# Kernel tuning notes

Measured on AMD Instinct MI355X. Metric: run time of the kernel, lower is better.

## Reference

```python
import jax, jax.numpy as jnp
import numpy as np

N_NODES = 100000
N_EDGES = 1600000
NUM_GRAPHS = 256


def _gcn_conv(x, src, dst, deg_isqrt, deg_inv, W, b):
    # GCNConv with self-loops and symmetric normalization (PyG semantics):
    # out_i = sum_{j->i} d_j^-1/2 d_i^-1/2 (x_j W) + d_i^-1 (x_i W) + b
    xl = x @ W  # [N, out]
    norm = deg_isqrt[src] * deg_isqrt[dst]  # [E]
    msgs = norm[:, None] * xl[src]  # [E, out] -- dominant memory traffic
    agg = jax.ops.segment_sum(msgs, dst, num_segments=N_NODES)
    return agg + deg_inv[:, None] * xl + b


def setup_inputs() -> dict:
    key = jax.random.key(0)
    ks = jax.random.split(key, 8)
    F_in, H, T = 128, 128, 64
    x = jax.random.normal(ks[0], (N_NODES, F_in), dtype=jnp.float32)
    edge_index = jax.random.randint(ks[1], (2, N_EDGES), 0, N_NODES, dtype=jnp.int64)
    batch = jnp.sort(jax.random.randint(ks[2], (N_NODES,), 0, NUM_GRAPHS, dtype=jnp.int64))
    s0 = 1.0 / np.sqrt(F_in)
    s1 = 1.0 / np.sqrt(H)
    return {
        "x": x,
        "edge_index": edge_index,
        "batch": batch,
        "W0": jax.random.normal(ks[3], (F_in, H), dtype=jnp.float32) * s0,
        "b0": jnp.zeros((H,), dtype=jnp.float32),
        "W1": jax.random.normal(ks[4], (H, H), dtype=jnp.float32) * s1,
        "b1": jnp.zeros((H,), dtype=jnp.float32),
        "W2": jax.random.normal(ks[5], (H, T), dtype=jnp.float32) * s1,
        "b2": jnp.zeros((T,), dtype=jnp.float32),
    }


def reference(x, edge_index, batch, W0, b0, W1, b1, W2, b2):
    src, dst = edge_index[0], edge_index[1]
    # degree including self-loop
    deg = jax.ops.segment_sum(jnp.ones((N_EDGES,), x.dtype), dst, num_segments=N_NODES) + 1.0
    deg_isqrt = jax.lax.rsqrt(deg)
    deg_inv = 1.0 / deg

    h = jax.nn.gelu(_gcn_conv(x, src, dst, deg_isqrt, deg_inv, W0, b0))
    h = jax.nn.gelu(_gcn_conv(h, src, dst, deg_isqrt, deg_inv, W1, b1))
    h = jax.nn.gelu(_gcn_conv(h, src, dst, deg_isqrt, deg_inv, W2, b2))

    # global_mean_pool over graphs
    sums = jax.ops.segment_sum(h, batch, num_segments=NUM_GRAPHS)
    counts = jax.ops.segment_sum(jnp.ones((N_NODES,), h.dtype), batch, num_segments=NUM_GRAPHS)
    return sums / jnp.maximum(counts, 1.0)[:, None]
```

## Files before the change

### kernel.cpp

```cpp
#include <hip/hip_runtime.h>
#include <math.h>

#define F_IN 128
#define TDIM 64
#define NGRAPH 256

typedef __attribute__((ext_vector_type(8))) short short8;
typedef __attribute__((ext_vector_type(4))) float f32x4;

__device__ __forceinline__ float gelu_f(float x) {
    float x3 = x * x * x;
    return 0.5f * x * (1.0f + tanhf(0.7978845608028654f * (x + 0.044715f * x3)));
}

__device__ __forceinline__ unsigned short bf16_of(float x) {
    unsigned u = __float_as_uint(x);
    return (unsigned short)((u + 0x7fffu + ((u >> 16) & 1u)) >> 16);
}
__device__ __forceinline__ float f_of(unsigned short h) {
    return __uint_as_float(((unsigned)h) << 16);
}
__device__ __forceinline__ unsigned bf16pair(float a, float b) {
    return (unsigned)bf16_of(a) | ((unsigned)bf16_of(b) << 16);
}
__device__ __forceinline__ float2 bf16unpack(unsigned u) {
    float2 r;
    r.x = __uint_as_float(u << 16);
    r.y = __uint_as_float(u & 0xffff0000u);
    return r;
}


#define BIN_CH 4096
#define MAXNB 512
#define CAP 6144

__global__ __launch_bounds__(256) void zero_kernel(float* __restrict__ psum,
                                                   float* __restrict__ pcnt,
                                                   int* __restrict__ bucket_cnt) {
    int i = blockIdx.x * 256 + threadIdx.x;
    if (i < NGRAPH * TDIM) psum[i] = 0.f;
    if (i < NGRAPH) pcnt[i] = 0.f;
    if (i < MAXNB) bucket_cnt[i] = 0;
}

__global__ __launch_bounds__(256) void binC_kernel(const int* __restrict__ src,
                                                   const int* __restrict__ dst,
                                                   int* __restrict__ bucket_cnt,
                                                   unsigned* __restrict__ tmp, int E, int NB) {
    __shared__ int hist[MAXNB];
    __shared__ int hbase[MAXNB];
    __shared__ int hcur[MAXNB];
    int tid = threadIdx.x;
    int base = blockIdx.x * BIN_CH;
    int end = base + BIN_CH;
    if (end > E) end = E;
    for (int i = tid; i < NB; i += 256) hist[i] = 0;
    __syncthreads();
    for (int e = base + tid; e < end; e += 256) atomicAdd(&hist[dst[e] >> 8], 1);
    __syncthreads();
    for (int i = tid; i < NB; i += 256) {
        int c = hist[i];
        hbase[i] = (c > 0) ? atomicAdd(&bucket_cnt[i], c) : 0;
        hcur[i] = 0;
    }
    __syncthreads();
    for (int e = base + tid; e < end; e += 256) {
        int d = dst[e];
        int b = d >> 8;
        int p = atomicAdd(&hcur[b], 1);
        int slot = hbase[b] + p;
        if (slot < CAP)
            tmp[(size_t)b * CAP + slot] = (unsigned)src[e] | ((unsigned)(d & 255) << 24);
    }
}

__global__ __launch_bounds__(256) void scan_wconv_kernel(const int* __restrict__ bucket_cnt,
                                                         int* __restrict__ bbase,
                                                         int* __restrict__ row_off, int NB,
                                                         int N, const float* __restrict__ W0,
                                                         const float* __restrict__ W1,
                                                         const float* __restrict__ W2,
                                                         unsigned short* __restrict__ hi0,
                                                         unsigned short* __restrict__ lo0,
                                                         unsigned short* __restrict__ hi1,
                                                         unsigned short* __restrict__ lo1,
                                                         unsigned short* __restrict__ hi2,
                                                         unsigned short* __restrict__ lo2) {
    if (blockIdx.x == 0) {
        if (threadIdx.x == 0) {
            int c = 0;
            for (int i = 0; i < NB; ++i) {
                bbase[i] = c;
                int v = bucket_cnt[i];
                c += (v < CAP ? v : CAP);
            }
            row_off[N] = c;
        }
        return;
    }
    int idx = (blockIdx.x - 1) * 256 + threadIdx.x;
    const float* W;
    unsigned short *whi, *wlo;
    int local, FOUT;
    if (idx < 16384) {
        W = W0; whi = hi0; wlo = lo0; local = idx; FOUT = 128;
    } else if (idx < 32768) {
        W = W1; whi = hi1; wlo = lo1; local = idx - 16384; FOUT = 128;
    } else if (idx < 40960) {
        W = W2; whi = hi2; wlo = lo2; local = idx - 32768; FOUT = 64;
    } else {
        return;
    }
    int k = local / FOUT;
    int n = local % FOUT;
    float w = W[local];
    unsigned short h = bf16_of(w);
    whi[(size_t)n * 128 + k] = h;
    wlo[(size_t)n * 128 + k] = bf16_of(w - f_of(h));
}

__global__ __launch_bounds__(256) void binDcount_kernel(const unsigned* __restrict__ tmp,
                                                        const int* __restrict__ bucket_cnt,
                                                        const int* __restrict__ bbase,
                                                        int* __restrict__ row_off,
                                                        float* __restrict__ isq,
                                                        float* __restrict__ dinv, int N) {
    __shared__ int lcnt[256];
    __shared__ int sh[256];
    int b = blockIdx.x;
    int tid = threadIdx.x;
    int cntb = bucket_cnt[b];
    if (cntb > CAP) cntb = CAP;
    lcnt[tid] = 0;
    __syncthreads();
    const unsigned* tb = tmp + (size_t)b * CAP;
    for (int e = tid; e < cntb; e += 256) atomicAdd(&lcnt[tb[e] >> 24], 1);
    __syncthreads();
    int own = lcnt[tid];
    sh[tid] = own;
    __syncthreads();
    for (int off = 1; off < 256; off <<= 1) {
        int x = (tid >= off) ? sh[tid - off] : 0;
        __syncthreads();
        sh[tid] += x;
        __syncthreads();
    }
    int excl = sh[tid] - own;
    int node = (b << 8) + tid;
    if (node < N) {
        row_off[node] = bbase[b] + excl;
        float d = (float)own + 1.0f;
        isq[node] = rsqrtf(d);
        dinv[node] = 1.0f / d;
    }
}

__global__ __launch_bounds__(256) void binDscatter_kernel(const unsigned* __restrict__ tmp,
                                                          const int* __restrict__ bucket_cnt,
                                                          const int* __restrict__ row_off,
                                                          const float* __restrict__ isq,
                                                          uint2* __restrict__ edges, int N) {
    __shared__ int lcur[256];
    __shared__ float lisq[256];
    int b = blockIdx.x;
    int node0 = b << 8;
    int tid = threadIdx.x;
    lcur[tid] = 0;
    int nd = node0 + tid;
    lisq[tid] = (nd < N) ? isq[nd] : 0.f;
    __syncthreads();
    int cntb = bucket_cnt[b];
    if (cntb > CAP) cntb = CAP;
    const unsigned* tb = tmp + (size_t)b * CAP;
    for (int e = tid; e < cntb; e += 256) {
        unsigned rec = tb[e];
        int dl = (int)(rec >> 24);
        unsigned s = rec & 0xFFFFFFu;
        int p = atomicAdd(&lcur[dl], 1);
        float nrm = isq[s] * lisq[dl];
        edges[(size_t)row_off[node0 + dl] + p] = make_uint2(s, __float_as_uint(nrm));
    }
}


#define LROW 136

__global__ __launch_bounds__(256) void gemm_f32_kernel(const float* __restrict__ X,
                                                       const unsigned short* __restrict__ whiT,
                                                       const unsigned short* __restrict__ wloT,
                                                       unsigned* __restrict__ Yb, int nrows) {
    constexpr int FOUT = 128;
    constexpr int NT = FOUT / 16;
    __shared__ short lds[2 * FOUT * LROW];
    short* shi = lds;
    short* slo = lds + FOUT * LROW;

    for (int c = threadIdx.x; c < FOUT * 16; c += 256) {
        int n = c >> 4, r = c & 15;
        *(short8*)(shi + n * LROW + r * 8) = *(const short8*)(whiT + (size_t)n * 128 + r * 8);
        *(short8*)(slo + n * LROW + r * 8) = *(const short8*)(wloT + (size_t)n * 128 + r * 8);
    }
    __syncthreads();

    int lane = threadIdx.x & 63;
    int wave = threadIdx.x >> 6;
    int quad = lane >> 4;
    int l16 = lane & 15;
    int rowBase = blockIdx.x * 256 + wave * 64;

    f32x4 acc[4][NT];
#pragma unroll
    for (int m = 0; m < 4; ++m)
#pragma unroll
        for (int t = 0; t < NT; ++t) acc[m][t] = (f32x4){0.f, 0.f, 0.f, 0.f};

    const float* xr[4];
    bool ok[4];
#pragma unroll
    for (int m = 0; m < 4; ++m) {
        int arow = rowBase + m * 16 + l16;
        ok[m] = arow < nrows;
        xr[m] = X + (size_t)arow * 128;
    }

#pragma unroll
    for (int k0 = 0; k0 < 128; k0 += 32) {
        short8 ahi[4], alo[4];
#pragma unroll
        for (int m = 0; m < 4; ++m) {
            float xv[8];
            if (ok[m]) {
                float4 v0 = *(const float4*)(xr[m] + k0 + quad * 8);
                float4 v1 = *(const float4*)(xr[m] + k0 + quad * 8 + 4);
                xv[0] = v0.x; xv[1] = v0.y; xv[2] = v0.z; xv[3] = v0.w;
                xv[4] = v1.x; xv[5] = v1.y; xv[6] = v1.z; xv[7] = v1.w;
            } else {
#pragma unroll
                for (int j = 0; j < 8; ++j) xv[j] = 0.f;
            }
#pragma unroll
            for (int j = 0; j < 8; ++j) {
                unsigned short h = bf16_of(xv[j]);
                ahi[m][j] = (short)h;
                alo[m][j] = (short)bf16_of(xv[j] - f_of(h));
            }
        }
#pragma unroll
        for (int t = 0; t < NT; ++t) {
            int off = (t * 16 + l16) * LROW + k0 + quad * 8;
            short8 bhi = *(const short8*)(shi + off);
            short8 blo = *(const short8*)(slo + off);
#pragma unroll
            for (int m = 0; m < 4; ++m) {
                acc[m][t] = __builtin_amdgcn_mfma_f32_16x16x32_bf16(ahi[m], bhi, acc[m][t], 0, 0, 0);
                acc[m][t] = __builtin_amdgcn_mfma_f32_16x16x32_bf16(alo[m], bhi, acc[m][t], 0, 0, 0);
                acc[m][t] = __builtin_amdgcn_mfma_f32_16x16x32_bf16(ahi[m], blo, acc[m][t], 0, 0, 0);
            }
        }
    }

#pragma unroll
    for (int m = 0; m < 4; ++m) {
#pragma unroll
        for (int t = 0; t < NT; ++t) {
            int col = t * 16 + l16;
#pragma unroll
            for (int i = 0; i < 4; ++i) {
                int r = rowBase + m * 16 + quad * 4 + i;
                float v = acc[m][t][i];
                float nb = __shfl_xor(v, 1, 64);
                if (((lane & 1) == 0) && r < nrows)
                    Yb[(size_t)r * (FOUT / 2) + (col >> 1)] = bf16pair(v, nb);
            }
        }
    }
}


template <int FOUT>
__global__ __launch_bounds__(256) void gemm_bf16_kernel(const unsigned* __restrict__ Xb,
                                                        const unsigned short* __restrict__ whiT,
                                                        unsigned* __restrict__ Yb, int nrows) {
    constexpr int NT = FOUT / 16;
    __shared__ short shi[FOUT * LROW];

    for (int c = threadIdx.x; c < FOUT * 16; c += 256) {
        int n = c >> 4, r = c & 15;
        *(short8*)(shi + n * LROW + r * 8) = *(const short8*)(whiT + (size_t)n * 128 + r * 8);
    }
    __syncthreads();

    int lane = threadIdx.x & 63;
    int wave = threadIdx.x >> 6;
    int quad = lane >> 4;
    int l16 = lane & 15;
    int rowBase = blockIdx.x * 256 + wave * 64;

    f32x4 acc[4][NT];
#pragma unroll
    for (int m = 0; m < 4; ++m)
#pragma unroll
        for (int t = 0; t < NT; ++t) acc[m][t] = (f32x4){0.f, 0.f, 0.f, 0.f};

    const short* xs[4];
    bool ok[4];
#pragma unroll
    for (int m = 0; m < 4; ++m) {
        int arow = rowBase + m * 16 + l16;
        ok[m] = arow < nrows;
        xs[m] = (const short*)Xb + (size_t)arow * 128;
    }

#pragma unroll
    for (int k0 = 0; k0 < 128; k0 += 32) {
        short8 a[4];
#pragma unroll
        for (int m = 0; m < 4; ++m) {
            if (ok[m])
                a[m] = *(const short8*)(xs[m] + k0 + quad * 8);
            else
                a[m] = (short8){0, 0, 0, 0, 0, 0, 0, 0};
        }
#pragma unroll
        for (int t = 0; t < NT; ++t) {
            short8 b = *(const short8*)(shi + (t * 16 + l16) * LROW + k0 + quad * 8);
#pragma unroll
            for (int m = 0; m < 4; ++m)
                acc[m][t] = __builtin_amdgcn_mfma_f32_16x16x32_bf16(a[m], b, acc[m][t], 0, 0, 0);
        }
    }

#pragma unroll
    for (int m = 0; m < 4; ++m) {
#pragma unroll
        for (int t = 0; t < NT; ++t) {
            int col = t * 16 + l16;
#pragma unroll
            for (int i = 0; i < 4; ++i) {
                int r = rowBase + m * 16 + quad * 4 + i;
                float v = acc[m][t][i];
                float nb = __shfl_xor(v, 1, 64);
                if (((lane & 1) == 0) && r < nrows)
                    Yb[(size_t)r * (FOUT / 2) + (col >> 1)] = bf16pair(v, nb);
            }
        }
    }
}


__global__ __launch_bounds__(256) void agg128_kernel(const unsigned* __restrict__ xlb,
                                                     const int* __restrict__ row_off,
                                                     const uint2* __restrict__ edges,
                                                     const float* __restrict__ dinv,
                                                     const float* __restrict__ bias,
                                                     unsigned* __restrict__ outb, int nnodes) {
    int wave = (blockIdx.x * blockDim.x + threadIdx.x) >> 6;
    int lane = threadIdx.x & 63;
    if (wave >= nnodes) return;
    int e0 = __builtin_amdgcn_readfirstlane(row_off[wave]);
    int e1 = __builtin_amdgcn_readfirstlane(row_off[wave + 1]);
    float ax = 0.f, ay = 0.f;
    int e = e0;
    int nfull = (e1 - e0) >> 4;
    for (int r = 0; r < nfull; ++r, e += 16) {
        uint2 edv = edges[e + (lane & 15)];
        unsigned sx[16];
        float nw[16];
#pragma unroll
        for (int j = 0; j < 16; ++j) {
            sx[j] = (unsigned)__builtin_amdgcn_readlane((int)edv.x, j);
            nw[j] = __uint_as_float((unsigned)__builtin_amdgcn_readlane((int)edv.y, j));
        }
        unsigned v[16];
#pragma unroll
        for (int j = 0; j < 16; ++j) v[j] = xlb[(size_t)sx[j] * 64 + lane];
#pragma unroll
        for (int j = 0; j < 16; ++j) {
            float2 f = bf16unpack(v[j]);
            ax += nw[j] * f.x;
            ay += nw[j] * f.y;
        }
    }
    if (e < e1) {
        int idx = e + (lane & 15);
        int cl = idx < e1 ? idx : e1 - 1;
        uint2 edv = edges[cl];
        unsigned sx[16];
        float nw[16];
#pragma unroll
        for (int j = 0; j < 16; ++j) {
            sx[j] = (unsigned)__builtin_amdgcn_readlane((int)edv.x, j);
            unsigned ny = (unsigned)__builtin_amdgcn_readlane((int)edv.y, j);
            nw[j] = (e + j < e1) ? __uint_as_float(ny) : 0.f;
        }
        unsigned v[16];
#pragma unroll
        for (int j = 0; j < 16; ++j) v[j] = xlb[(size_t)sx[j] * 64 + lane];
#pragma unroll
        for (int j = 0; j < 16; ++j) {
            float2 f = bf16unpack(v[j]);
            ax += nw[j] * f.x;
            ay += nw[j] * f.y;
        }
    }
    float di = dinv[wave];
    float2 pi = bf16unpack(xlb[(size_t)wave * 64 + lane]);
    float2 bb = *(const float2*)(bias + lane * 2);
    outb[(size_t)wave * 64 + lane] =
        bf16pair(gelu_f(ax + di * pi.x + bb.x), gelu_f(ay + di * pi.y + bb.y));
}


__global__ __launch_bounds__(256) void agg64_kernel(const unsigned* __restrict__ xlb,
                                                    const int* __restrict__ row_off,
                                                    const uint2* __restrict__ edges,
                                                    const float* __restrict__ dinv,
                                                    const float* __restrict__ bias,
                                                    unsigned* __restrict__ outb, int nnodes) {
    int wave = (blockIdx.x * blockDim.x + threadIdx.x) >> 6;
    int lane = threadIdx.x & 63;
    int sub = lane >> 5;
    int sl = lane & 31;
    int node = wave * 2 + sub;
    bool nv = node < nnodes;
    int e0 = nv ? row_off[node] : 0;
    int e1 = nv ? row_off[node + 1] : 0;
    int rounds = (e1 - e0 + 15) >> 4;
    int ro = __shfl_xor(rounds, 32, 64);
    int maxr = rounds > ro ? rounds : ro;
    float ax = 0.f, ay = 0.f;
    for (int r = 0; r < maxr; ++r) {
        int base = e0 + (r << 4);
        uint2 ed[16];
#pragma unroll
        for (int j = 0; j < 16; ++j) {
            int idx = base + j;
            int cl = idx < e1 ? idx : (e1 > e0 ? e1 - 1 : 0);
            ed[j] = edges[cl];
            if (idx >= e1) ed[j].y = 0u;
        }
        unsigned v[16];
#pragma unroll
        for (int j = 0; j < 16; ++j) v[j] = xlb[(size_t)ed[j].x * 32 + sl];
#pragma unroll
        for (int j = 0; j < 16; ++j) {
            float nw = __uint_as_float(ed[j].y);
            float2 f = bf16unpack(v[j]);
            ax += nw * f.x;
            ay += nw * f.y;
        }
    }
    if (nv) {
        float di = dinv[node];
        float2 pi = bf16unpack(xlb[(size_t)node * 32 + sl]);
        float2 bb = *(const float2*)(bias + sl * 2);
        outb[(size_t)node * 32 + sl] =
            bf16pair(gelu_f(ax + di * pi.x + bb.x), gelu_f(ay + di * pi.y + bb.y));
    }
}


#define POOL_CHUNK 64

__global__ __launch_bounds__(256) void pool_kernel(const unsigned* __restrict__ hb,
                                                   const int* __restrict__ batch,
                                                   float* __restrict__ psum,
                                                   float* __restrict__ pcnt, int nnodes) {
    int wave = (blockIdx.x * blockDim.x + threadIdx.x) >> 6;
    int lane = threadIdx.x & 63;
    int half = lane >> 5;
    int p = lane & 31;
    int n0 = wave * POOL_CHUNK + half * 32;
    if (n0 >= nnodes) return;
    int n1 = n0 + 32;
    if (n1 > nnodes) n1 = nnodes;

    int g_cur = batch[n0];
    float accx = 0.f, accy = 0.f;
    int cnt = 0;
    for (int node = n0; node < n1; ++node) {
        int g = batch[node];
        if (g != g_cur) {
            atomicAdd(&psum[g_cur * TDIM + 2 * p], accx);
            atomicAdd(&psum[g_cur * TDIM + 2 * p + 1], accy);
            if (p == 0) atomicAdd(&pcnt[g_cur], (float)cnt);
            accx = 0.f;
            accy = 0.f;
            cnt = 0;
            g_cur = g;
        }
        float2 f = bf16unpack(hb[(size_t)node * 32 + p]);
        accx += f.x;
        accy += f.y;
        ++cnt;
    }
    atomicAdd(&psum[g_cur * TDIM + 2 * p], accx);
    atomicAdd(&psum[g_cur * TDIM + 2 * p + 1], accy);
    if (p == 0) atomicAdd(&pcnt[g_cur], (float)cnt);
}

__global__ __launch_bounds__(256) void fin_kernel(const float* __restrict__ psum,
                                                  const float* __restrict__ pcnt,
                                                  float* __restrict__ out) {
    int i = blockIdx.x * blockDim.x + threadIdx.x;
    if (i < NGRAPH * TDIM) {
        float c = pcnt[i >> 6];
        out[i] = psum[i] / fmaxf(c, 1.0f);
    }
}


extern "C" void kernel_launch(void* const* d_in, const int* in_sizes, int n_in,
                              void* d_out, int out_size, void* d_ws, size_t ws_size,
                              hipStream_t stream) {
    const float* x = (const float*)d_in[0];
    const int* ei = (const int*)d_in[1];
    const int* batch = (const int*)d_in[2];
    const float* W0 = (const float*)d_in[3];
    const float* b0 = (const float*)d_in[4];
    const float* W1 = (const float*)d_in[5];
    const float* b1 = (const float*)d_in[6];
    const float* W2 = (const float*)d_in[7];
    const float* b2 = (const float*)d_in[8];

    const int N = in_sizes[0] / F_IN;
    const int E = in_sizes[1] / 2;
    const int* src = ei;
    const int* dst = ei + E;
    const int NB = (N + 255) >> 8;

    char* w = (char*)d_ws;
    auto alloc = [&](size_t bytes) -> void* {
        void* p = (void*)w;
        w += (bytes + 255) & ~(size_t)255;
        return p;
    };
    float* isq = (float*)alloc((size_t)N * 4);
    float* dinv = (float*)alloc((size_t)N * 4);
    int* bucket_cnt = (int*)alloc((size_t)MAXNB * 4);
    int* bbase = (int*)alloc((size_t)MAXNB * 4);
    int* row_off = (int*)alloc((size_t)(N + 1) * 4);
    uint2* edges = (uint2*)alloc((size_t)E * 8);
    unsigned* tmp = (unsigned*)alloc((size_t)NB * CAP * 4);
    float* psum = (float*)alloc((size_t)NGRAPH * TDIM * 4);
    float* pcnt = (float*)alloc((size_t)NGRAPH * 4);
    unsigned* bufXb = (unsigned*)alloc((size_t)N * 64 * 4);
    unsigned* bufHb = (unsigned*)alloc((size_t)N * 64 * 4);
    unsigned short* whiT0 = (unsigned short*)alloc(128 * 128 * 2);
    unsigned short* wloT0 = (unsigned short*)alloc(128 * 128 * 2);
    unsigned short* whiT1 = (unsigned short*)alloc(128 * 128 * 2);
    unsigned short* wloT1 = (unsigned short*)alloc(128 * 128 * 2);
    unsigned short* whiT2 = (unsigned short*)alloc(64 * 128 * 2);
    unsigned short* wloT2 = (unsigned short*)alloc(64 * 128 * 2);

    zero_kernel<<<(NGRAPH * TDIM + 255) / 256, 256, 0, stream>>>(psum, pcnt, bucket_cnt);

    int cblocks = (E + BIN_CH - 1) / BIN_CH;
    binC_kernel<<<cblocks, 256, 0, stream>>>(src, dst, bucket_cnt, tmp, E, NB);
    scan_wconv_kernel<<<1 + (40960 + 255) / 256, 256, 0, stream>>>(
        bucket_cnt, bbase, row_off, NB, N, W0, W1, W2, whiT0, wloT0, whiT1, wloT1, whiT2,
        wloT2);
    binDcount_kernel<<<NB, 256, 0, stream>>>(tmp, bucket_cnt, bbase, row_off, isq, dinv, N);
    binDscatter_kernel<<<NB, 256, 0, stream>>>(tmp, bucket_cnt, row_off, isq, edges, N);

    int gblocks = (N + 255) / 256;
    int ablocks = (N * 64 + 255) / 256;
    int a64blocks = (((N + 1) / 2) * 64 + 255) / 256;

    gemm_f32_kernel<<<gblocks, 256, 0, stream>>>(x, whiT0, wloT0, bufXb, N);
    agg128_kernel<<<ablocks, 256, 0, stream>>>(bufXb, row_off, edges, dinv, b0, bufHb, N);
    gemm_bf16_kernel<128><<<gblocks, 256, 0, stream>>>(bufHb, whiT1, bufXb, N);
    agg128_kernel<<<ablocks, 256, 0, stream>>>(bufXb, row_off, edges, dinv, b1, bufHb, N);
    gemm_bf16_kernel<64><<<gblocks, 256, 0, stream>>>(bufHb, whiT2, bufXb, N);
    agg64_kernel<<<a64blocks, 256, 0, stream>>>(bufXb, row_off, edges, dinv, b2, bufHb, N);

    int pwaves = (N + POOL_CHUNK - 1) / POOL_CHUNK;
    int pblocks = (pwaves * 64 + 255) / 256;
    pool_kernel<<<pblocks, 256, 0, stream>>>(bufHb, batch, psum, pcnt, N);
    fin_kernel<<<(NGRAPH * TDIM + 255) / 256, 256, 0, stream>>>(psum, pcnt, (float*)d_out);
}
```

Baseline: 432.9 us.

## Store GEMM outputs as fp16 and aggregate with fused mixed-precision FMA

GEMM outputs (xl) are now packed as fp16 instead of bf16, and the aggregation kernels consume them with v_fma_mix_f32, which converts and fuses the multiply-add in one instruction. Edge metadata is broadcast with ds_bpermute rather than readlane for the weights, and agg64 loads one coalesced edge vector per round instead of sixteen per-lane edge loads. The bucket prefix scan becomes a parallel block scan instead of a single-thread serial loop. fp16 gives more mantissa but less range than bf16, so large activations could overflow, and the scan assumes NB is at most 512.

```diff
diff --git a/kernel.cpp b/kernel.cpp
--- a/kernel.cpp
+++ b/kernel.cpp
@@ -7,6 +7,7 @@
 
 typedef __attribute__((ext_vector_type(8))) short short8;
 typedef __attribute__((ext_vector_type(4))) float f32x4;
+typedef __attribute__((ext_vector_type(2))) __fp16 fp16x2;
 
 __device__ __forceinline__ float gelu_f(float x) {
     float x3 = x * x * x;
@@ -28,6 +29,27 @@
     r.x = __uint_as_float(u << 16);
     r.y = __uint_as_float(u & 0xffff0000u);
     return r;
+}
+
+__device__ __forceinline__ unsigned pkf16(float a, float b) {
+    fp16x2 h = __builtin_amdgcn_cvt_pkrtz(a, b);
+    return __builtin_bit_cast(unsigned, h);
+}
+__device__ __forceinline__ float2 f16unpack(unsigned u) {
+    fp16x2 h = __builtin_bit_cast(fp16x2, u);
+    float2 r;
+    r.x = (float)h[0];
+    r.y = (float)h[1];
+    return r;
+}
+
+__device__ __forceinline__ void fmix2(float& ax, float& ay, unsigned pk, float nw) {
+    asm("v_fma_mix_f32 %0, %1, %2, %0 op_sel:[0,0,0] op_sel_hi:[1,0,0]"
+        : "+v"(ax)
+        : "v"(pk), "v"(nw));
+    asm("v_fma_mix_f32 %0, %1, %2, %0 op_sel:[1,0,0] op_sel_hi:[1,0,0]"
+        : "+v"(ay)
+        : "v"(pk), "v"(nw));
 }
 
 
@@ -88,15 +110,31 @@
                                                          unsigned short* __restrict__ hi2,
                                                          unsigned short* __restrict__ lo2) {
     if (blockIdx.x == 0) {
-        if (threadIdx.x == 0) {
-            int c = 0;
-            for (int i = 0; i < NB; ++i) {
-                bbase[i] = c;
-                int v = bucket_cnt[i];
-                c += (v < CAP ? v : CAP);
-            }
-            row_off[N] = c;
-        }
+        __shared__ int sh[256];
+        int tid = threadIdx.x;
+        int i0 = tid * 2;
+        int v0 = 0, v1 = 0;
+        if (i0 < NB) {
+            v0 = bucket_cnt[i0];
+            v0 = v0 < CAP ? v0 : CAP;
+        }
+        if (i0 + 1 < NB) {
+            v1 = bucket_cnt[i0 + 1];
+            v1 = v1 < CAP ? v1 : CAP;
+        }
+        int s = v0 + v1;
+        sh[tid] = s;
+        __syncthreads();
+        for (int off = 1; off < 256; off <<= 1) {
+            int x = (tid >= off) ? sh[tid - off] : 0;
+            __syncthreads();
+            sh[tid] += x;
+            __syncthreads();
+        }
+        int excl = sh[tid] - s;
+        if (i0 < NB) bbase[i0] = excl;
+        if (i0 + 1 < NB) bbase[i0 + 1] = excl + v0;
+        if (tid == 255) row_off[N] = sh[255];
         return;
     }
     int idx = (blockIdx.x - 1) * 256 + threadIdx.x;
@@ -271,7 +309,7 @@
                 float v = acc[m][t][i];
                 float nb = __shfl_xor(v, 1, 64);
                 if (((lane & 1) == 0) && r < nrows)
-                    Yb[(size_t)r * (FOUT / 2) + (col >> 1)] = bf16pair(v, nb);
+                    Yb[(size_t)r * (FOUT / 2) + (col >> 1)] = pkf16(v, nb);
             }
         }
     }
@@ -342,7 +380,7 @@
                 float v = acc[m][t][i];
                 float nb = __shfl_xor(v, 1, 64);
                 if (((lane & 1) == 0) && r < nrows)
-                    Yb[(size_t)r * (FOUT / 2) + (col >> 1)] = bf16pair(v, nb);
+                    Yb[(size_t)r * (FOUT / 2) + (col >> 1)] = pkf16(v, nb);
             }
         }
     }
@@ -362,50 +400,38 @@
     int e1 = __builtin_amdgcn_readfirstlane(row_off[wave + 1]);
     float ax = 0.f, ay = 0.f;
     int e = e0;
+    int l16 = lane & 15;
     int nfull = (e1 - e0) >> 4;
     for (int r = 0; r < nfull; ++r, e += 16) {
-        uint2 edv = edges[e + (lane & 15)];
-        unsigned sx[16];
+        uint2 edv = edges[e + l16];
+        unsigned pk[16];
         float nw[16];
 #pragma unroll
         for (int j = 0; j < 16; ++j) {
-            sx[j] = (unsigned)__builtin_amdgcn_readlane((int)edv.x, j);
-            nw[j] = __uint_as_float((unsigned)__builtin_amdgcn_readlane((int)edv.y, j));
-        }
-        unsigned v[16];
-#pragma unroll
-        for (int j = 0; j < 16; ++j) v[j] = xlb[(size_t)sx[j] * 64 + lane];
+            int sx = __builtin_amdgcn_readlane((int)edv.x, j);
+            nw[j] = __uint_as_float((unsigned)__builtin_amdgcn_ds_bpermute(j * 4, (int)edv.y));
+            pk[j] = xlb[(size_t)(unsigned)sx * 64 + lane];
+        }
+#pragma unroll
+        for (int j = 0; j < 16; ++j) fmix2(ax, ay, pk[j], nw[j]);
+    }
+    if (e < e1) {
+        int idx = e + l16;
+        uint2 edv = edges[idx < e1 ? idx : e1 - 1];
+        if (idx >= e1) edv.y = 0u;
+        unsigned pk[16];
+        float nw[16];
 #pragma unroll
         for (int j = 0; j < 16; ++j) {
-            float2 f = bf16unpack(v[j]);
-            ax += nw[j] * f.x;
-            ay += nw[j] * f.y;
-        }
-    }
-    if (e < e1) {
-        int idx = e + (lane & 15);
-        int cl = idx < e1 ? idx : e1 - 1;
-        uint2 edv = edges[cl];
-        unsigned sx[16];
-        float nw[16];
-#pragma unroll
-        for (int j = 0; j < 16; ++j) {
-            sx[j] = (unsigned)__builtin_amdgcn_readlane((int)edv.x, j);
-            unsigned ny = (unsigned)__builtin_amdgcn_readlane((int)edv.y, j);
-            nw[j] = (e + j < e1) ? __uint_as_float(ny) : 0.f;
-        }
-        unsigned v[16];
-#pragma unroll
-        for (int j = 0; j < 16; ++j) v[j] = xlb[(size_t)sx[j] * 64 + lane];
-#pragma unroll
-        for (int j = 0; j < 16; ++j) {
-            float2 f = bf16unpack(v[j]);
-            ax += nw[j] * f.x;
-            ay += nw[j] * f.y;
-        }
+            int sx = __builtin_amdgcn_readlane((int)edv.x, j);
+            nw[j] = __uint_as_float((unsigned)__builtin_amdgcn_ds_bpermute(j * 4, (int)edv.y));
+            pk[j] = xlb[(size_t)(unsigned)sx * 64 + lane];
+        }
+#pragma unroll
+        for (int j = 0; j < 16; ++j) fmix2(ax, ay, pk[j], nw[j]);
     }
     float di = dinv[wave];
-    float2 pi = bf16unpack(xlb[(size_t)wave * 64 + lane]);
+    float2 pi = f16unpack(xlb[(size_t)wave * 64 + lane]);
     float2 bb = *(const float2*)(bias + lane * 2);
     outb[(size_t)wave * 64 + lane] =
         bf16pair(gelu_f(ax + di * pi.x + bb.x), gelu_f(ay + di * pi.y + bb.y));
@@ -430,30 +456,29 @@
     int ro = __shfl_xor(rounds, 32, 64);
     int maxr = rounds > ro ? rounds : ro;
     float ax = 0.f, ay = 0.f;
+    int bidx = (lane & 32) << 2;
     for (int r = 0; r < maxr; ++r) {
-        int base = e0 + (r << 4);
-        uint2 ed[16];
+        int idx = e0 + (r << 4) + (lane & 15);
+        int cl = idx < e1 ? idx : (e1 > e0 ? e1 - 1 : 0);
+        uint2 edv = edges[cl];
+        if (idx >= e1) edv.y = 0u;
+        int sv[16];
+        float nw[16];
 #pragma unroll
         for (int j = 0; j < 16; ++j) {
-            int idx = base + j;
-            int cl = idx < e1 ? idx : (e1 > e0 ? e1 - 1 : 0);
-            ed[j] = edges[cl];
-            if (idx >= e1) ed[j].y = 0u;
-        }
-        unsigned v[16];
-#pragma unroll
-        for (int j = 0; j < 16; ++j) v[j] = xlb[(size_t)ed[j].x * 32 + sl];
-#pragma unroll
-        for (int j = 0; j < 16; ++j) {
-            float nw = __uint_as_float(ed[j].y);
-            float2 f = bf16unpack(v[j]);
-            ax += nw * f.x;
-            ay += nw * f.y;
-        }
+            int bj = bidx + j * 4;
+            sv[j] = __builtin_amdgcn_ds_bpermute(bj, (int)edv.x);
+            nw[j] = __uint_as_float((unsigned)__builtin_amdgcn_ds_bpermute(bj, (int)edv.y));
+        }
+        unsigned pk[16];
+#pragma unroll
+        for (int j = 0; j < 16; ++j) pk[j] = xlb[(((unsigned)sv[j]) << 5) + (unsigned)sl];
+#pragma unroll
+        for (int j = 0; j < 16; ++j) fmix2(ax, ay, pk[j], nw[j]);
     }
     if (nv) {
         float di = dinv[node];
-        float2 pi = bf16unpack(xlb[(size_t)node * 32 + sl]);
+        float2 pi = f16unpack(xlb[(size_t)node * 32 + sl]);
         float2 bb = *(const float2*)(bias + sl * 2);
         outb[(size_t)node * 32 + sl] =
             bf16pair(gelu_f(ax + di * pi.x + bb.x), gelu_f(ay + di * pi.y + bb.y));
```

Result: faster. 386.8 us (-10.7%).
